# Optimization experiments

Hardware: AMD Instinct MI355X
Metric: run time of the kernel (lower is better)

Reference implementation:

```python
import jax, jax.numpy as jnp
import numpy as np

NUM_HEAD = 8
GN_GROUPS = 32
EPS = 1e-5


def group_norm(x, w, b):
    # x: [B,C,H,W]; GroupNorm over 32 groups
    B, C, H, W = x.shape
    xg = x.reshape(B, GN_GROUPS, C // GN_GROUPS, H, W)
    mu = jnp.mean(xg, axis=(2, 3, 4), keepdims=True)
    var = jnp.var(xg, axis=(2, 3, 4), keepdims=True)
    xn = ((xg - mu) * jax.lax.rsqrt(var + EPS)).reshape(B, C, H, W)
    return xn * w[None, :, None, None] + b[None, :, None, None]


def conv1x1(x, w, b):
    # 1x1 conv == channel-wise linear: w [O,C], x [B,C,H,W]
    return jnp.einsum('oc,bchw->bohw', w, x) + b[None, :, None, None]


def setup_inputs() -> dict:
    key = jax.random.key(0)
    ks = jax.random.split(key, 6)
    B, C, H, W = 8, 512, 32, 32
    s = 1.0 / np.sqrt(C)
    return {
        'x': jax.random.normal(ks[0], (B, C, H, W), jnp.float32),
        'gn_w': jnp.ones((C,), jnp.float32),
        'gn_b': jnp.zeros((C,), jnp.float32),
        'wq': jax.random.normal(ks[1], (C, C), jnp.float32) * s,
        'bq': jnp.zeros((C,), jnp.float32),
        'wk': jax.random.normal(ks[2], (C, C), jnp.float32) * s,
        'bk': jnp.zeros((C,), jnp.float32),
        'wv': jax.random.normal(ks[3], (C, C), jnp.float32) * s,
        'bv': jnp.zeros((C,), jnp.float32),
        'wo': jax.random.normal(ks[4], (C, C), jnp.float32) * s,
        'bo': jnp.zeros((C,), jnp.float32),
    }


def reference(x, gn_w, gn_b, wq, bq, wk, bk, wv, bv, wo, bo):
    B, C, H, W = x.shape
    Hn = NUM_HEAD
    d = C // Hn
    N = H * W
    scale = d ** -0.5

    xn = group_norm(x, gn_w, gn_b)
    q = conv1x1(xn, wq, bq).reshape(B, Hn, d, N)  # [B,Hn,d,N]
    k = conv1x1(xn, wk, bk).reshape(B, Hn, d, N)
    v = conv1x1(xn, wv, bv).reshape(B, Hn, d, N)

    # attn[b,h,i,j] = sum_d q[b,h,d,i] * k[b,h,d,j]
    attn = jnp.einsum('bhdi,bhdj->bhij', q, k) * scale
    attn = jax.nn.softmax(attn, axis=-1)
    # out[b,h,d,i] = sum_j attn[b,h,i,j] * v[b,h,d,j]
    out = jnp.einsum('bhij,bhdj->bhdi', attn, v).reshape(B, C, H, W)
    return x + conv1x1(out, wo, bo)
```

## Files before the change

### kernel.cpp

```cpp
#include <hip/hip_runtime.h>
#include <hip/hip_bf16.h>

typedef unsigned short ushort_t;
typedef __bf16 bf16_t;
typedef bf16_t bf16x8 __attribute__((ext_vector_type(8)));
typedef float f32x4 __attribute__((ext_vector_type(4)));
typedef float f32x16 __attribute__((ext_vector_type(16)));

#define CH 512
#define NSP 1024

__device__ __forceinline__ float bf2f(ushort_t u) {
    union { unsigned int i; float f; } t; t.i = ((unsigned int)u) << 16; return t.f;
}
__device__ __forceinline__ ushort_t f2bf(float f) {
    union { float fl; unsigned int i; } t; t.fl = f;
    unsigned int r = t.i + 0x7fffu + ((t.i >> 16) & 1u);
    return (ushort_t)(r >> 16);
}
__device__ __forceinline__ unsigned int pk2(float a, float b) {
    __hip_bfloat162 h = __float22bfloat162_rn(make_float2(a, b));
    union { __hip_bfloat162 h2; unsigned int u; } t; t.h2 = h; return t.u;
}

#if __has_builtin(__builtin_amdgcn_global_load_lds)
#define HAVE_ASYNC_LDS 1
#endif
__device__ __forceinline__ void cp16(const ushort_t* g, ushort_t* l) {
#ifdef HAVE_ASYNC_LDS
    __builtin_amdgcn_global_load_lds((const __attribute__((address_space(1))) unsigned int*)g,
                                     (__attribute__((address_space(3))) unsigned int*)l, 16, 0, 0);
#else
    *(uint4*)l = *(const uint4*)g;
#endif
}

#if __has_builtin(__builtin_amdgcn_exp2f)
#define EXP2(x) __builtin_amdgcn_exp2f(x)
#else
#define EXP2(x) exp2f(x)
#endif

#define QSCALE 0.18033688011112042f

__global__ __launch_bounds__(256) void prep_kernel(const float* __restrict__ x,
                                                   const float* __restrict__ w0, const float* __restrict__ w1,
                                                   const float* __restrict__ w2, const float* __restrict__ w3,
                                                   float2* __restrict__ gstats, ushort_t* __restrict__ wbf) {
    int tid = threadIdx.x;
    if (blockIdx.x >= 256) {
        int idx = (blockIdx.x - 256) * 256 + tid;
        int my = idx >> 16;
        const float* src = (my == 0) ? w0 : (my == 1) ? w1 : (my == 2) ? w2 : w3;
        float4 v = reinterpret_cast<const float4*>(src)[idx & 65535];
        uint2 u = make_uint2(pk2(v.x, v.y), pk2(v.z, v.w));
        reinterpret_cast<uint2*>(wbf + (size_t)my * 262144)[idx & 65535] = u;
        return;
    }
    __shared__ float red[8];
    int bg = blockIdx.x;
    size_t base = (size_t)bg * 16384;
    float s = 0.f, s2 = 0.f;
    const float4* x4 = reinterpret_cast<const float4*>(x + base);
    for (int i = tid; i < 4096; i += 256) {
        float4 v = x4[i];
        s  += v.x + v.y + v.z + v.w;
        s2 += v.x * v.x + v.y * v.y + v.z * v.z + v.w * v.w;
    }
    #pragma unroll
    for (int off = 32; off > 0; off >>= 1) {
        s  += __shfl_down(s, off, 64);
        s2 += __shfl_down(s2, off, 64);
    }
    int wv = tid >> 6;
    if ((tid & 63) == 0) { red[wv] = s; red[4 + wv] = s2; }
    __syncthreads();
    if (tid == 0) {
        float ts  = red[0] + red[1] + red[2] + red[3];
        float ts2 = red[4] + red[5] + red[6] + red[7];
        float mu  = ts * (1.f / 16384.f);
        float var = ts2 * (1.f / 16384.f) - mu * mu;
        gstats[bg] = make_float2(mu, rsqrtf(var + 1e-5f));
    }
}

__global__ __launch_bounds__(256) void gn_apply(const float* __restrict__ x, const float* __restrict__ gw,
                                                const float* __restrict__ gbias, const float2* __restrict__ gstats,
                                                ushort_t* __restrict__ xnt) {
    __shared__ __align__(16) ushort_t lt[16 * 264];
    int nq = blockIdx.x;
    int bg = blockIdx.y;
    int b = bg >> 5, g = bg & 31;
    int tid = threadIdx.x;
    float2 st = gstats[bg];
    float mu = st.x, rstd = st.y;
    const float4* x4 = reinterpret_cast<const float4*>(x + ((size_t)(b * 512 + g * 16) * 1024 + nq * 256));
    #pragma unroll
    for (int rep = 0; rep < 4; rep++) {
        int id = rep * 256 + tid;
        int cc = id >> 6, j = id & 63;
        float ww = gw[g * 16 + cc], bb = gbias[g * 16 + cc];
        float ca = rstd * ww, cb = bb - mu * ca;
        float4 v = x4[cc * 256 + j];
        uint2 u = make_uint2(pk2(v.x * ca + cb, v.y * ca + cb), pk2(v.z * ca + cb, v.w * ca + cb));
        *reinterpret_cast<uint2*>(&lt[cc * 264 + j * 4]) = u;
    }
    __syncthreads();
    int n = tid;
    ushort_t ov[16];
    #pragma unroll
    for (int cc = 0; cc < 16; cc++) ov[cc] = lt[cc * 264 + n];
    ushort_t* dst = xnt + ((size_t)(b * 1024 + nq * 256 + n)) * 512 + g * 16;
    *reinterpret_cast<ushort4*>(dst + 0)  = *reinterpret_cast<ushort4*>(&ov[0]);
    *reinterpret_cast<ushort4*>(dst + 4)  = *reinterpret_cast<ushort4*>(&ov[4]);
    *reinterpret_cast<ushort4*>(dst + 8)  = *reinterpret_cast<ushort4*>(&ov[8]);
    *reinterpret_cast<ushort4*>(dst + 12) = *reinterpret_cast<ushort4*>(&ov[12]);
}

__global__ __launch_bounds__(256) void conv_qkv(const ushort_t* __restrict__ xnt,
                                                const ushort_t* __restrict__ wbf,
                                                const float* __restrict__ bq,
                                                const float* __restrict__ bk,
                                                const float* __restrict__ bv,
                                                ushort_t* __restrict__ qt,
                                                ushort_t* __restrict__ kt,
                                                ushort_t* __restrict__ vt) {
    __shared__ __align__(16) char smem[16384];
    ushort_t* als = (ushort_t*)smem;
    ushort_t* bls = (ushort_t*)(smem + 8192);
    int tid = threadIdx.x;
    int wave = tid >> 6, lane = tid & 63, l15 = lane & 15, quad = lane >> 4;
    int wm = wave >> 1, wn = wave & 1;
    int m0 = blockIdx.x * 128, o0 = blockIdx.y * 128, b = blockIdx.z;
    const ushort_t* A = xnt + (size_t)b * 524288;

    f32x4 acc[4][4];
    #pragma unroll
    for (int ms = 0; ms < 4; ms++)
        #pragma unroll
        for (int ns = 0; ns < 4; ns++) acc[ms][ns] = (f32x4){0.f, 0.f, 0.f, 0.f};

    for (int k0 = 0; k0 < 512; k0 += 32) {
        #pragma unroll
        for (int rep = 0; rep < 2; rep++) {
            int id = rep * 256 + tid;
            int r = id >> 2, part = id & 3;
            int sw = part ^ ((r >> 2) & 3);
            cp16(A + (size_t)(m0 + r) * 512 + k0 + sw * 8, als + (size_t)id * 8);
            cp16(wbf + (size_t)(o0 + r) * 512 + k0 + sw * 8, bls + (size_t)id * 8);
        }
        __syncthreads();
        bf16x8 af[4], bfr[4];
        #pragma unroll
        for (int ms = 0; ms < 4; ms++) {
            int row = wm * 64 + ms * 16 + l15;
            int slot = quad ^ ((row >> 2) & 3);
            af[ms] = *(const bf16x8*)(als + row * 32 + slot * 8);
        }
        #pragma unroll
        for (int ns = 0; ns < 4; ns++) {
            int row = wn * 64 + ns * 16 + l15;
            int slot = quad ^ ((row >> 2) & 3);
            bfr[ns] = *(const bf16x8*)(bls + row * 32 + slot * 8);
        }
        #pragma unroll
        for (int ms = 0; ms < 4; ms++)
            #pragma unroll
            for (int ns = 0; ns < 4; ns++)
                acc[ms][ns] = __builtin_amdgcn_mfma_f32_16x16x32_bf16(af[ms], bfr[ns], acc[ms][ns], 0, 0, 0);
        __syncthreads();
    }

    int seg = o0 >> 9, lo = o0 & 511;
    if (seg < 2) {
        const float* bias = seg ? bk : bq;
        ushort_t* dst = seg ? kt : qt;
        float s = seg ? 1.f : QSCALE;
        ushort_t* cls = (ushort_t*)smem;
        #pragma unroll
        for (int oh = 0; oh < 2; oh++) {
            if (oh) __syncthreads();
            if (wn == oh) {
                #pragma unroll
                for (int ns = 0; ns < 4; ns++) {
                    float bb = bias[lo + oh * 64 + ns * 16 + l15];
                    #pragma unroll
                    for (int ms = 0; ms < 4; ms++) {
                        int idx = (wm * 64 + ms * 16 + quad * 4) * 64 + ns * 16 + l15;
                        unsigned ua = pk2((acc[ms][ns][0] + bb) * s, (acc[ms][ns][1] + bb) * s);
                        unsigned ub = pk2((acc[ms][ns][2] + bb) * s, (acc[ms][ns][3] + bb) * s);
                        cls[idx]       = (ushort_t)(ua & 0xffff);
                        cls[idx + 64]  = (ushort_t)(ua >> 16);
                        cls[idx + 128] = (ushort_t)(ub & 0xffff);
                        cls[idx + 192] = (ushort_t)(ub >> 16);
                    }
                }
            }
            __syncthreads();
            int h = (lo >> 6) + oh;
            size_t obase = ((size_t)(b * 8 + h) * 1024 + m0) * 64;
            #pragma unroll
            for (int rep = 0; rep < 4; rep++) {
                int idd = rep * 256 + tid;
                int r = idd >> 3, part = idd & 7;
                *(uint4*)(dst + obase + (size_t)r * 64 + part * 8) = *(const uint4*)(cls + r * 64 + part * 8);
            }
        }
    } else {
        #pragma unroll
        for (int ns = 0; ns < 4; ns++) {
            int c = lo + wn * 64 + ns * 16 + l15;
            float bb = bv[c];
            #pragma unroll
            for (int ms = 0; ms < 4; ms++) {
                int n = m0 + wm * 64 + ms * 16 + quad * 4;
                uint2 u = make_uint2(pk2(acc[ms][ns][0] + bb, acc[ms][ns][1] + bb),
                                     pk2(acc[ms][ns][2] + bb, acc[ms][ns][3] + bb));
                *(uint2*)(vt + ((size_t)(b * 512 + c)) * 1024 + n) = u;
            }
        }
    }
}

#define Z16 {0.f,0.f,0.f,0.f,0.f,0.f,0.f,0.f,0.f,0.f,0.f,0.f,0.f,0.f,0.f,0.f}

#define PV_STEP(JS, P) {                                                                     \
    unsigned wA0 = pk2(P[((JS)&1)*8+0], P[((JS)&1)*8+1]);                                    \
    unsigned wA1 = pk2(P[((JS)&1)*8+2], P[((JS)&1)*8+3]);                                    \
    unsigned wB0 = pk2(P[((JS)&1)*8+4], P[((JS)&1)*8+5]);                                    \
    unsigned wB1 = pk2(P[((JS)&1)*8+6], P[((JS)&1)*8+7]);                                    \
    asm("v_permlane32_swap_b32 %0, %1" : "+v"(wA0), "+v"(wB0));                              \
    asm("v_permlane32_swap_b32 %0, %1" : "+v"(wA1), "+v"(wB1));                              \
    union { unsigned u[4]; bf16x8 v; } pa_;                                                  \
    pa_.u[0] = wA0; pa_.u[1] = wA1; pa_.u[2] = wB0; pa_.u[3] = wB1;                          \
    int phys_ = (((JS) * 2) | hi) ^ r7;                                                      \
    bf16x8 vf0 = *(const bf16x8*)(vbuf + l31 * 64 + phys_ * 8);                              \
    bf16x8 vf1 = *(const bf16x8*)(vbuf + (32 + l31) * 64 + phys_ * 8);                       \
    __builtin_amdgcn_s_setprio(1);                                                           \
    vacc0 = __builtin_amdgcn_mfma_f32_32x32x16_bf16(pa_.v, vf0, vacc0, 0, 0, 0);             \
    vacc1 = __builtin_amdgcn_mfma_f32_32x32x16_bf16(pa_.v, vf1, vacc1, 0, 0, 0);             \
    __builtin_amdgcn_s_setprio(0); }

__global__ __launch_bounds__(256) void attn_kernel(const ushort_t* __restrict__ qt,
                                                   const ushort_t* __restrict__ kt,
                                                   const ushort_t* __restrict__ vt,
                                                   ushort_t* __restrict__ ao) {
    __shared__ __align__(16) ushort_t smem[16384];
    int tid = threadIdx.x;
    int wave = tid >> 6, lane = tid & 63, l31 = lane & 31, hi = lane >> 5;
    int id = blockIdx.x;
    int bh = (id & 7) * 8 + (id >> 6);
    int i0 = ((id >> 3) & 7) * 128;
    const ushort_t* qb = qt + (size_t)bh * 65536;
    const ushort_t* kb = kt + (size_t)bh * 65536;
    const ushort_t* vb = vt + (size_t)bh * 65536;
    int iw0 = i0 + wave * 32;
    int r7 = l31 & 7;

    bf16x8 qf[4];
    #pragma unroll
    for (int ks = 0; ks < 4; ks++)
        qf[ks] = *(const bf16x8*)(qb + (size_t)(iw0 + l31) * 64 + ks * 16 + hi * 8);

    f32x16 vacc0 = Z16, vacc1 = Z16;
    float lacc = 0.f;

    int rk0 = tid >> 3, sk = tid & 7, rk1 = rk0 + 32;
    const ushort_t* kg0 = kb + rk0 * 64 + (sk ^ (rk0 & 7)) * 8;
    const ushort_t* kg1 = kb + rk1 * 64 + (sk ^ (rk1 & 7)) * 8;
    const ushort_t* vg0 = vb + (size_t)rk0 * 1024 + (sk ^ (rk0 & 7)) * 8;
    const ushort_t* vg1 = vb + (size_t)rk1 * 1024 + (sk ^ (rk1 & 7)) * 8;

    cp16(kg0, smem + tid * 8);
    cp16(kg1, smem + (tid + 256) * 8);
    cp16(vg0, smem + 8192 + tid * 8);
    cp16(vg1, smem + 8192 + (tid + 256) * 8);
    kg0 += 4096; kg1 += 4096; vg0 += 64; vg1 += 64;
    __syncthreads();

    for (int jt = 0; jt < 16; jt++) {
        int cur = jt & 1;
        if (jt < 15) {
            ushort_t* kd = smem + (cur ^ 1) * 4096;
            ushort_t* vd = smem + 8192 + (cur ^ 1) * 4096;
            cp16(kg0, kd + tid * 8);
            cp16(kg1, kd + (tid + 256) * 8);
            cp16(vg0, vd + tid * 8);
            cp16(vg1, vd + (tid + 256) * 8);
            kg0 += 4096; kg1 += 4096; vg0 += 64; vg1 += 64;
        }
        const ushort_t* kbuf = smem + cur * 4096;
        const ushort_t* vbuf = smem + 8192 + cur * 4096;

        f32x16 s0 = Z16, s1 = Z16;
        __builtin_amdgcn_s_setprio(1);
        #pragma unroll
        for (int ks = 0; ks < 4; ks++) {
            int phys = ((ks * 2) | hi) ^ r7;
            bf16x8 kf = *(const bf16x8*)(kbuf + l31 * 64 + phys * 8);
            s0 = __builtin_amdgcn_mfma_f32_32x32x16_bf16(kf, qf[ks], s0, 0, 0, 0);
        }
        #pragma unroll
        for (int ks = 0; ks < 4; ks++) {
            int phys = ((ks * 2) | hi) ^ r7;
            bf16x8 kf = *(const bf16x8*)(kbuf + (32 + l31) * 64 + phys * 8);
            s1 = __builtin_amdgcn_mfma_f32_32x32x16_bf16(kf, qf[ks], s1, 0, 0, 0);
        }
        __builtin_amdgcn_s_setprio(0);

        float p0[16], p1[16];
        #pragma unroll
        for (int r = 0; r < 16; r++) p0[r] = EXP2(s0[r]);
        #pragma unroll
        for (int r = 0; r < 16; r++) p1[r] = EXP2(s1[r]);
        float t0 = 0.f, t1 = 0.f, t2 = 0.f, t3 = 0.f;
        #pragma unroll
        for (int r = 0; r < 4; r++) { t0 += p0[r]; t1 += p0[4 + r]; t2 += p0[8 + r]; t3 += p0[12 + r]; }
        #pragma unroll
        for (int r = 0; r < 4; r++) { t0 += p1[r]; t1 += p1[4 + r]; t2 += p1[8 + r]; t3 += p1[12 + r]; }
        lacc += (t0 + t1) + (t2 + t3);

        PV_STEP(0, p0)
        PV_STEP(1, p0)
        PV_STEP(2, p1)
        PV_STEP(3, p1)

        __syncthreads();
    }

    lacc += __shfl_xor(lacc, 32, 64);
    float linv[16];
    #pragma unroll
    for (int r = 0; r < 16; r++) {
        int ir = (r & 3) + 8 * (r >> 2) + 4 * hi;
        linv[r] = 1.f / __shfl(lacc, ir, 64);
    }

    ushort_t* ols = smem;
    #pragma unroll
    for (int r = 0; r < 16; r++) {
        int irow = wave * 32 + (r & 3) + 8 * (r >> 2) + 4 * hi;
        ols[irow * 80 + l31]      = f2bf(vacc0[r] * linv[r]);
        ols[irow * 80 + 32 + l31] = f2bf(vacc1[r] * linv[r]);
    }
    __syncthreads();
    int b = bh >> 3, h = bh & 7;
    ushort_t* aob = ao + ((size_t)b * 1024 + i0) * 512 + h * 64;
    #pragma unroll
    for (int rep = 0; rep < 4; rep++) {
        int idd = rep * 256 + tid;
        int rl = idd >> 3, part = idd & 7;
        *(uint4*)(aob + (size_t)rl * 512 + part * 8) = *(const uint4*)(ols + rl * 80 + part * 8);
    }
}

__global__ __launch_bounds__(256) void conv_out(const ushort_t* __restrict__ ao,
                                                const ushort_t* __restrict__ wo,
                                                const float* __restrict__ bo,
                                                const float* __restrict__ xres,
                                                float* __restrict__ out) {
    __shared__ __align__(16) char smem[16384];
    ushort_t* als = (ushort_t*)smem;
    ushort_t* bls = (ushort_t*)(smem + 8192);
    int tid = threadIdx.x;
    int wave = tid >> 6, lane = tid & 63, l15 = lane & 15, quad = lane >> 4;
    int wm = wave >> 1, wn = wave & 1;
    int m0 = blockIdx.x * 128, o0 = blockIdx.y * 128, b = blockIdx.z;
    const ushort_t* A = ao + (size_t)b * 524288;

    f32x4 acc[4][4];
    #pragma unroll
    for (int ms = 0; ms < 4; ms++)
        #pragma unroll
        for (int ns = 0; ns < 4; ns++) acc[ms][ns] = (f32x4){0.f, 0.f, 0.f, 0.f};

    for (int k0 = 0; k0 < 512; k0 += 32) {
        #pragma unroll
        for (int rep = 0; rep < 2; rep++) {
            int id = rep * 256 + tid;
            int r = id >> 2, part = id & 3;
            int sw = part ^ ((r >> 2) & 3);
            cp16(A + (size_t)(m0 + r) * 512 + k0 + sw * 8, als + (size_t)id * 8);
            cp16(wo + (size_t)(o0 + r) * 512 + k0 + sw * 8, bls + (size_t)id * 8);
        }
        __syncthreads();
        bf16x8 af[4], bfr[4];
        #pragma unroll
        for (int ms = 0; ms < 4; ms++) {
            int row = wm * 64 + ms * 16 + l15;
            int slot = quad ^ ((row >> 2) & 3);
            af[ms] = *(const bf16x8*)(als + row * 32 + slot * 8);
        }
        #pragma unroll
        for (int ns = 0; ns < 4; ns++) {
            int row = wn * 64 + ns * 16 + l15;
            int slot = quad ^ ((row >> 2) & 3);
            bfr[ns] = *(const bf16x8*)(bls + row * 32 + slot * 8);
        }
        #pragma unroll
        for (int ms = 0; ms < 4; ms++)
            #pragma unroll
            for (int ns = 0; ns < 4; ns++)
                acc[ms][ns] = __builtin_amdgcn_mfma_f32_16x16x32_bf16(af[ms], bfr[ns], acc[ms][ns], 0, 0, 0);
        __syncthreads();
    }

    #pragma unroll
    for (int ns = 0; ns < 4; ns++) {
        int o = o0 + wn * 64 + ns * 16 + l15;
        float bb = bo[o];
        #pragma unroll
        for (int ms = 0; ms < 4; ms++) {
            int n = m0 + wm * 64 + ms * 16 + quad * 4;
            size_t ga = ((size_t)(b * 512 + o)) * 1024 + n;
            float4 xv = *(const float4*)(xres + ga);
            float4 c4;
            c4.x = acc[ms][ns][0] + bb + xv.x;
            c4.y = acc[ms][ns][1] + bb + xv.y;
            c4.z = acc[ms][ns][2] + bb + xv.z;
            c4.w = acc[ms][ns][3] + bb + xv.w;
            *(float4*)(out + ga) = c4;
        }
    }
}

extern "C" void kernel_launch(void* const* d_in, const int* in_sizes, int n_in,
                              void* d_out, int out_size, void* d_ws, size_t ws_size,
                              hipStream_t stream) {
    const float* x    = (const float*)d_in[0];
    const float* gn_w = (const float*)d_in[1];
    const float* gn_b = (const float*)d_in[2];
    const float* wq   = (const float*)d_in[3];
    const float* bq   = (const float*)d_in[4];
    const float* wk   = (const float*)d_in[5];
    const float* bk   = (const float*)d_in[6];
    const float* wv   = (const float*)d_in[7];
    const float* bv   = (const float*)d_in[8];
    const float* wo   = (const float*)d_in[9];
    const float* bo   = (const float*)d_in[10];

    char* ws = (char*)d_ws;
    ushort_t* xnt  = (ushort_t*)(ws);
    ushort_t* qt   = (ushort_t*)(ws + (((size_t)8)  << 20));
    ushort_t* kt   = (ushort_t*)(ws + (((size_t)16) << 20));
    ushort_t* vt   = (ushort_t*)(ws + (((size_t)24) << 20));
    ushort_t* wbf  = (ushort_t*)(ws + (((size_t)32) << 20));
    float2*   gst  = (float2*)  (ws + (((size_t)34) << 20));
    ushort_t* ao   = xnt;

    prep_kernel<<<1280, 256, 0, stream>>>(x, wq, wk, wv, wo, gst, wbf);
    gn_apply<<<dim3(4, 256), 256, 0, stream>>>(x, gn_w, gn_b, gst, xnt);

    conv_qkv<<<dim3(8, 12, 8), 256, 0, stream>>>(xnt, wbf, bq, bk, bv, qt, kt, vt);

    attn_kernel<<<512, 256, 0, stream>>>(qt, kt, vt, ao);

    conv_out<<<dim3(8, 4, 8), 256, 0, stream>>>(ao, wbf + 786432, bo, x, (float*)d_out);
}
```

Before: 174.4 us.

## Split PV accumulators and retile output conv to 64x64 with LDS-staged epilogue

The attention kernel now spreads the P·V MFMA chain over two pairs of accumulators, which breaks the serial dependency between back-to-back MFMAs, and sums them once after the loop. The output 1x1 conv switches from 128x128 to 64x64 tiles, giving four times as many blocks (1024), and swaps the operand roles so weights index output channels. Its results go through shared memory so the bias-plus-residual epilogue writes fully coalesced float4 rows. The cost is more accumulator registers in attention, and in the conv less operand reuse per block plus an extra LDS round trip.

New measurement: 171.5 us. No clear change (-1.7%).

```diff
diff --git a/kernel.cpp b/kernel.cpp
--- a/kernel.cpp
+++ b/kernel.cpp
@@ -224,7 +224,7 @@
 
 #define Z16 {0.f,0.f,0.f,0.f,0.f,0.f,0.f,0.f,0.f,0.f,0.f,0.f,0.f,0.f,0.f,0.f}
 
-#define PV_STEP(JS, P) {                                                                     \
+#define PV_STEP(JS, P, VA, VB) {                                                             \
     unsigned wA0 = pk2(P[((JS)&1)*8+0], P[((JS)&1)*8+1]);                                    \
     unsigned wA1 = pk2(P[((JS)&1)*8+2], P[((JS)&1)*8+3]);                                    \
     unsigned wB0 = pk2(P[((JS)&1)*8+4], P[((JS)&1)*8+5]);                                    \
@@ -237,8 +237,8 @@
     bf16x8 vf0 = *(const bf16x8*)(vbuf + l31 * 64 + phys_ * 8);                              \
     bf16x8 vf1 = *(const bf16x8*)(vbuf + (32 + l31) * 64 + phys_ * 8);                       \
     __builtin_amdgcn_s_setprio(1);                                                           \
-    vacc0 = __builtin_amdgcn_mfma_f32_32x32x16_bf16(pa_.v, vf0, vacc0, 0, 0, 0);             \
-    vacc1 = __builtin_amdgcn_mfma_f32_32x32x16_bf16(pa_.v, vf1, vacc1, 0, 0, 0);             \
+    VA = __builtin_amdgcn_mfma_f32_32x32x16_bf16(pa_.v, vf0, VA, 0, 0, 0);                   \
+    VB = __builtin_amdgcn_mfma_f32_32x32x16_bf16(pa_.v, vf1, VB, 0, 0, 0);                   \
     __builtin_amdgcn_s_setprio(0); }
 
 __global__ __launch_bounds__(256) void attn_kernel(const ushort_t* __restrict__ qt,
@@ -262,7 +262,7 @@
     for (int ks = 0; ks < 4; ks++)
         qf[ks] = *(const bf16x8*)(qb + (size_t)(iw0 + l31) * 64 + ks * 16 + hi * 8);
 
-    f32x16 vacc0 = Z16, vacc1 = Z16;
+    f32x16 vacc0a = Z16, vacc0b = Z16, vacc1a = Z16, vacc1b = Z16;
     float lacc = 0.f;
 
     int rk0 = tid >> 3, sk = tid & 7, rk1 = rk0 + 32;
@@ -320,13 +320,16 @@
         for (int r = 0; r < 4; r++) { t0 += p1[r]; t1 += p1[4 + r]; t2 += p1[8 + r]; t3 += p1[12 + r]; }
         lacc += (t0 + t1) + (t2 + t3);
 
-        PV_STEP(0, p0)
-        PV_STEP(1, p0)
-        PV_STEP(2, p1)
-        PV_STEP(3, p1)
+        PV_STEP(0, p0, vacc0a, vacc1a)
+        PV_STEP(1, p0, vacc0b, vacc1b)
+        PV_STEP(2, p1, vacc0a, vacc1a)
+        PV_STEP(3, p1, vacc0b, vacc1b)
 
         __syncthreads();
     }
+
+    f32x16 vacc0 = vacc0a + vacc0b;
+    f32x16 vacc1 = vacc1a + vacc1b;
 
     lacc += __shfl_xor(lacc, 32, 64);
     float linv[16];
@@ -359,68 +362,69 @@
                                                 const float* __restrict__ bo,
                                                 const float* __restrict__ xres,
                                                 float* __restrict__ out) {
-    __shared__ __align__(16) char smem[16384];
+    __shared__ __align__(16) char smem[17408];
     ushort_t* als = (ushort_t*)smem;
-    ushort_t* bls = (ushort_t*)(smem + 8192);
+    ushort_t* bls = (ushort_t*)(smem + 4096);
     int tid = threadIdx.x;
     int wave = tid >> 6, lane = tid & 63, l15 = lane & 15, quad = lane >> 4;
     int wm = wave >> 1, wn = wave & 1;
-    int m0 = blockIdx.x * 128, o0 = blockIdx.y * 128, b = blockIdx.z;
-    const ushort_t* A = ao + (size_t)b * 524288;
-
-    f32x4 acc[4][4];
-    #pragma unroll
-    for (int ms = 0; ms < 4; ms++)
-        #pragma unroll
-        for (int ns = 0; ns < 4; ns++) acc[ms][ns] = (f32x4){0.f, 0.f, 0.f, 0.f};
+    int m0 = blockIdx.x * 64, n0 = blockIdx.y * 64, b = blockIdx.z;
+    const ushort_t* B = ao + (size_t)b * 524288;
+
+    f32x4 acc[2][2];
+    #pragma unroll
+    for (int ms = 0; ms < 2; ms++)
+        #pragma unroll
+        for (int ns = 0; ns < 2; ns++) acc[ms][ns] = (f32x4){0.f, 0.f, 0.f, 0.f};
 
     for (int k0 = 0; k0 < 512; k0 += 32) {
-        #pragma unroll
-        for (int rep = 0; rep < 2; rep++) {
-            int id = rep * 256 + tid;
-            int r = id >> 2, part = id & 3;
+        {
+            int r = tid >> 2, part = tid & 3;
             int sw = part ^ ((r >> 2) & 3);
-            cp16(A + (size_t)(m0 + r) * 512 + k0 + sw * 8, als + (size_t)id * 8);
-            cp16(wo + (size_t)(o0 + r) * 512 + k0 + sw * 8, bls + (size_t)id * 8);
+            cp16(wo + (size_t)(m0 + r) * 512 + k0 + sw * 8, als + (size_t)tid * 8);
+            cp16(B + (size_t)(n0 + r) * 512 + k0 + sw * 8, bls + (size_t)tid * 8);
         }
         __syncthreads();
-        bf16x8 af[4], bfr[4];
-        #pragma unroll
-        for (int ms = 0; ms < 4; ms++) {
-            int row = wm * 64 + ms * 16 + l15;
+        bf16x8 af[2], bfr[2];
+        #pragma unroll
+        for (int ms = 0; ms < 2; ms++) {
+            int row = wm * 32 + ms * 16 + l15;
             int slot = quad ^ ((row >> 2) & 3);
             af[ms] = *(const bf16x8*)(als + row * 32 + slot * 8);
         }
         #pragma unroll
-        for (int ns = 0; ns < 4; ns++) {
-            int row = wn * 64 + ns * 16 + l15;
+        for (int ns = 0; ns < 2; ns++) {
+            int row = wn * 32 + ns * 16 + l15;
             int slot = quad ^ ((row >> 2) & 3);
             bfr[ns] = *(const bf16x8*)(bls + row * 32 + slot * 8);
         }
         #pragma unroll
-        for (int ms = 0; ms < 4; ms++)
+        for (int ms = 0; ms < 2; ms++)
             #pragma unroll
-            for (int ns = 0; ns < 4; ns++)
+            for (int ns = 0; ns < 2; ns++)
                 acc[ms][ns] = __builtin_amdgcn_mfma_f32_16x16x32_bf16(af[ms], bfr[ns], acc[ms][ns], 0, 0, 0);
         __syncthreads();
     }
 
-    #pragma unroll
-    for (int ns = 0; ns < 4; ns++) {
-        int o = o0 + wn * 64 + ns * 16 + l15;
-        float bb = bo[o];
-        #pragma unroll
-        for (int ms = 0; ms < 4; ms++) {
-            int n = m0 + wm * 64 + ms * 16 + quad * 4;
-            size_t ga = ((size_t)(b * 512 + o)) * 1024 + n;
-            float4 xv = *(const float4*)(xres + ga);
-            float4 c4;
-            c4.x = acc[ms][ns][0] + bb + xv.x;
-            c4.y = acc[ms][ns][1] + bb + xv.y;
-            c4.z = acc[ms][ns][2] + bb + xv.z;
-            c4.w = acc[ms][ns][3] + bb + xv.w;
-            *(float4*)(out + ga) = c4;
-        }
+    float* clsf = (float*)smem;
+    #pragma unroll
+    for (int ms = 0; ms < 2; ms++)
+        #pragma unroll
+        for (int ns = 0; ns < 2; ns++)
+            #pragma unroll
+            for (int r = 0; r < 4; r++)
+                clsf[(wm * 32 + ms * 16 + quad * 4 + r) * 68 + wn * 32 + ns * 16 + l15] = acc[ms][ns][r];
+    __syncthreads();
+    #pragma unroll
+    for (int rep = 0; rep < 4; rep++) {
+        int id = rep * 256 + tid;
+        int row = id >> 4, part = id & 15;
+        float bvr = bo[m0 + row];
+        float4 c4 = *(const float4*)(clsf + row * 68 + part * 4);
+        size_t ga = ((size_t)(b * 512 + m0 + row)) * 1024 + n0 + part * 4;
+        float4 xv = *(const float4*)(xres + ga);
+        c4.x += bvr + xv.x; c4.y += bvr + xv.y; c4.z += bvr + xv.z; c4.w += bvr + xv.w;
+        *(float4*)(out + ga) = c4;
     }
 }
 
@@ -455,5 +459,5 @@
 
     attn_kernel<<<512, 256, 0, stream>>>(qt, kt, vt, ao);
 
-    conv_out<<<dim3(8, 4, 8), 256, 0, stream>>>(ao, wbf + 786432, bo, x, (float*)d_out);
-}
+    conv_out<<<dim3(8, 16, 8), 256, 0, stream>>>(ao, wbf + 786432, bo, x, (float*)d_out);
+}
```
